# Kernel tuning notes

Measured on AMD Instinct MI355X. Metric: run time of the kernel, lower is better.

Reference implementation:

```python
import jax, jax.numpy as jnp
import numpy as np

N_NODES = 100000
DROP_P = 0.2


def _degree_norm(idx, n):
    deg = jax.ops.segment_sum(jnp.ones_like(idx, dtype=jnp.float32), idx, num_segments=n)
    return jnp.maximum(deg, 1.0) ** -0.5


def gcn_layer(x, src, dst, W, b, n):
    # DGL GraphConv, norm='both', in_feats > out_feats so weight is applied first.
    norm_src = _degree_norm(src, n)  # out-degree^{-1/2}
    norm_dst = _degree_norm(dst, n)  # in-degree^{-1/2}
    h = (x * norm_src[:, None]) @ W            # [N, d_out]
    agg = jax.ops.segment_sum(h[src], dst, num_segments=n)  # gather-scatter over edges
    return agg * norm_dst[:, None] + b


def setup_inputs() -> dict:
    key = jax.random.key(0)
    k = jax.random.split(key, 5)
    x = jax.random.normal(k[0], (N_NODES, 256), dtype=jnp.float32)
    edge_index = jax.random.randint(k[1], (2, 1600000), 0, N_NODES, dtype=jnp.int64)
    W1 = jax.random.normal(k[2], (256, 128), dtype=jnp.float32) * (1.0 / np.sqrt(256))
    b1 = jnp.zeros((128,), dtype=jnp.float32)
    W2 = jax.random.normal(k[3], (128, 47), dtype=jnp.float32) * (1.0 / np.sqrt(128))
    b2 = jnp.zeros((47,), dtype=jnp.float32)
    return {"x": x, "edge_index": edge_index, "W1": W1, "b1": b1, "W2": W2, "b2": b2}


def reference(x, edge_index, W1, b1, W2, b2):
    src, dst = edge_index[0], edge_index[1]
    n = x.shape[0]
    # CRD: GraphConv -> relu -> dropout (F.dropout default training=True; fixed mask)
    h = gcn_layer(x, src, dst, W1, b1, n)
    h = jax.nn.relu(h)
    keep = jax.random.bernoulli(jax.random.key(42), 1.0 - DROP_P, h.shape)
    h = jnp.where(keep, h / (1.0 - DROP_P), 0.0)
    # CLS: GraphConv -> log_softmax over class dim
    out = gcn_layer(h, src, dst, W2, b2, n)
    return jax.nn.log_softmax(out, axis=-1)
```

## Files before the change

kernel.cpp:

```cpp
#include <hip/hip_runtime.h>
#include <math.h>


#define NF0 256
#define NF1 128
#define NC  47
#define CB  1024

typedef __attribute__((ext_vector_type(8))) short bfrag;
typedef __attribute__((ext_vector_type(4))) float f32x4;

__device__ __forceinline__ unsigned short f2bf(float f) {
  unsigned u = __float_as_uint(f);
  return (unsigned short)((u + 0x7fffu + ((u >> 16) & 1u)) >> 16);
}
__device__ __forceinline__ unsigned pack2bf(float a, float b) {
  return (unsigned)f2bf(a) | ((unsigned)f2bf(b) << 16);
}
__device__ __forceinline__ float bflo(unsigned v) { return __uint_as_float(v << 16); }
__device__ __forceinline__ float bfhi(unsigned v) { return __uint_as_float(v & 0xffff0000u); }
__device__ __forceinline__ float bf2f(unsigned short b) {
  return __uint_as_float((unsigned)b << 16);
}

__device__ __forceinline__ unsigned rotl_(unsigned x, int n) {
  return (x << n) | (x >> (32 - n));
}
__device__ __forceinline__ void threefry2x32_(unsigned x0, unsigned x1,
                                              unsigned& o0, unsigned& o1) {
  const unsigned k0 = 0u, k1 = 42u;
  const unsigned k2 = k0 ^ k1 ^ 0x1BD11BDAu;
  x0 += k0; x1 += k1;
  x0+=x1; x1=rotl_(x1,13); x1^=x0;
  x0+=x1; x1=rotl_(x1,15); x1^=x0;
  x0+=x1; x1=rotl_(x1,26); x1^=x0;
  x0+=x1; x1=rotl_(x1, 6); x1^=x0;
  x0+=k1; x1+=k2+1u;
  x0+=x1; x1=rotl_(x1,17); x1^=x0;
  x0+=x1; x1=rotl_(x1,29); x1^=x0;
  x0+=x1; x1=rotl_(x1,16); x1^=x0;
  x0+=x1; x1=rotl_(x1,24); x1^=x0;
  x0+=k2; x1+=k0+2u;
  x0+=x1; x1=rotl_(x1,13); x1^=x0;
  x0+=x1; x1=rotl_(x1,15); x1^=x0;
  x0+=x1; x1=rotl_(x1,26); x1^=x0;
  x0+=x1; x1=rotl_(x1, 6); x1^=x0;
  x0+=k0; x1+=k1+3u;
  x0+=x1; x1=rotl_(x1,17); x1^=x0;
  x0+=x1; x1=rotl_(x1,29); x1^=x0;
  x0+=x1; x1=rotl_(x1,16); x1^=x0;
  x0+=x1; x1=rotl_(x1,24); x1^=x0;
  x0+=k1; x1+=k2+4u;
  x0+=x1; x1=rotl_(x1,13); x1^=x0;
  x0+=x1; x1=rotl_(x1,15); x1^=x0;
  x0+=x1; x1=rotl_(x1,26); x1^=x0;
  x0+=x1; x1=rotl_(x1, 6); x1^=x0;
  x0+=k2; x1+=k0+5u;
  o0 = x0; o1 = x1;
}
__device__ __forceinline__ float dropout_mul(int j) {
  unsigned o0, o1;
  threefry2x32_(0u, (unsigned)j, o0, o1);
  unsigned bits = o0 ^ o1;
  float u = __uint_as_float((bits >> 9) | 0x3f800000u) - 1.0f;
  return (u < 0.8f) ? 1.25f : 0.0f;
}


__global__ __launch_bounds__(256) void k_chist(const int* __restrict__ ei, int E,
                                               int nbk,
                                               unsigned* __restrict__ bCntD,
                                               unsigned* __restrict__ bCntS,
                                               const float* __restrict__ W1,
                                               const float* __restrict__ W2,
                                               unsigned* __restrict__ W1t32,
                                               unsigned* __restrict__ W2t32) {
  if (blockIdx.x >= 256) {
    int i = (blockIdx.x - 256) * 256 + threadIdx.x;
    if (i < 128 * 128) {
      int n = i >> 7, k = (i & 127) << 1;
      W1t32[i] = pack2bf(W1[(size_t)k * NF1 + n], W1[(size_t)(k + 1) * NF1 + n]);
    } else if (i < 128 * 128 + 48 * 64) {
      int j = i - 128 * 128;
      int f = j >> 6, k = (j & 63) << 1;
      float a = (f < NC) ? W2[(size_t)k * NC + f] : 0.f;
      float c = (f < NC) ? W2[(size_t)(k + 1) * NC + f] : 0.f;
      W2t32[j] = pack2bf(a, c);
    }
    return;
  }
  __shared__ unsigned hd[128], hs[128];
  for (int i = threadIdx.x; i < 128; i += 256) { hd[i] = 0; hs[i] = 0; }
  __syncthreads();
  for (int e = blockIdx.x * 256 + threadIdx.x; e < E; e += 256 * 256) {
    int s = ei[e], d = ei[E + e];
    atomicAdd(&hs[s >> 10], 1u);
    atomicAdd(&hd[d >> 10], 1u);
  }
  __syncthreads();
  for (int i = threadIdx.x; i < nbk; i += 256) {
    if (hd[i]) atomicAdd(&bCntD[i], hd[i]);
    if (hs[i]) atomicAdd(&bCntS[i], hs[i]);
  }
}

__global__ __launch_bounds__(256) void k_cscatter(const int* __restrict__ ei, int E,
                                                  const unsigned* __restrict__ bCntD,
                                                  const unsigned* __restrict__ bCntS,
                                                  unsigned* __restrict__ curD,
                                                  unsigned* __restrict__ curS,
                                                  unsigned* __restrict__ pd,
                                                  unsigned short* __restrict__ ps,
                                                  int nbk) {
  __shared__ unsigned hd[128], hs[128];
  __shared__ unsigned baseD[128], baseS[128];
  __shared__ unsigned sc[256];
  const int t = threadIdx.x;
  int per = (E + gridDim.x - 1) / gridDim.x;
  int e0 = blockIdx.x * per;
  int e1 = min(e0 + per, E);
  unsigned orig = (t < 128) ? ((t < nbk) ? bCntD[t] : 0u)
                            : (((t - 128) < nbk) ? bCntS[t - 128] : 0u);
  sc[t] = orig;
  if (t < 128) { hd[t] = 0; hs[t] = 0; }
  __syncthreads();
  for (int e = e0 + t; e < e1; e += 256) {
    int s = ei[e], d = ei[E + e];
    atomicAdd(&hs[s >> 10], 1u);
    atomicAdd(&hd[d >> 10], 1u);
  }
  __syncthreads();
  #pragma unroll
  for (int o = 1; o < 128; o <<= 1) {
    unsigned u = ((t & 127) >= o) ? sc[t - o] : 0u;
    __syncthreads();
    sc[t] += u;
    __syncthreads();
  }
  if (t < 128) {
    unsigned excl = sc[t] - orig;
    unsigned h = hd[t];
    baseD[t] = excl + (h ? atomicAdd(&curD[t], h) : 0u);
    hd[t] = 0;
  } else {
    int i = t - 128;
    unsigned excl = sc[t] - orig;
    unsigned h = hs[i];
    baseS[i] = excl + (h ? atomicAdd(&curS[i], h) : 0u);
    hs[i] = 0;
  }
  __syncthreads();
  for (int e = e0 + t; e < e1; e += 256) {
    int s = ei[e], d = ei[E + e];
    int bd = d >> 10, bs = s >> 10;
    unsigned pD = baseD[bd] + atomicAdd(&hd[bd], 1u);
    unsigned pS = baseS[bs] + atomicAdd(&hs[bs], 1u);
    pd[pD] = ((unsigned)(d & (CB - 1)) << 17) | (unsigned)s;
    ps[pS] = (unsigned short)(s & (CB - 1));
  }
}

__global__ __launch_bounds__(256) void k_fine(const unsigned* __restrict__ bCntD,
                                              const unsigned* __restrict__ bCntS,
                                              const unsigned* __restrict__ pd,
                                              const unsigned short* __restrict__ ps,
                                              unsigned* __restrict__ off,
                                              float* __restrict__ norm_dst,
                                              float* __restrict__ norm_src,
                                              int* __restrict__ csr,
                                              int N, int E, int nbk) {
  __shared__ unsigned cnt[CB];
  __shared__ unsigned part[256];
  __shared__ unsigned sc[256];
  const int t = threadIdx.x;
  const bool isD = (int)blockIdx.x < nbk;
  const int b = isD ? (int)blockIdx.x : ((int)blockIdx.x - nbk);
  unsigned orig = (t < 128) ? ((t < nbk) ? bCntD[t] : 0u)
                            : (((t - 128) < nbk) ? bCntS[t - 128] : 0u);
  sc[t] = orig;
  __syncthreads();
  #pragma unroll
  for (int o = 1; o < 128; o <<= 1) {
    unsigned u = ((t & 127) >= o) ? sc[t - o] : 0u;
    __syncthreads();
    sc[t] += u;
    __syncthreads();
  }
  const int idx = isD ? b : (128 + b);
  const unsigned hi = sc[idx];
  const unsigned lo = hi - (isD ? bCntD[b] : bCntS[b]);
  const int base = b << 10;
  for (int i = t; i < CB; i += 256) cnt[i] = 0;
  __syncthreads();
  if (isD) {
    for (unsigned j = lo + t; j < hi; j += 256) atomicAdd(&cnt[pd[j] >> 17], 1u);
    __syncthreads();
    unsigned c0 = cnt[4*t], c1 = cnt[4*t+1], c2 = cnt[4*t+2], c3 = cnt[4*t+3];
    unsigned tsum = c0 + c1 + c2 + c3;
    part[t] = tsum;
    __syncthreads();
    #pragma unroll
    for (int o = 1; o < 256; o <<= 1) {
      unsigned u = (t >= o) ? part[t - o] : 0u;
      __syncthreads();
      part[t] += u;
      __syncthreads();
    }
    unsigned e0 = part[t] - tsum;
    unsigned p0 = e0, p1 = e0 + c0, p2 = p1 + c1, p3 = p2 + c2;
    int n0 = base + 4 * t;
    if (n0 + 0 < N) { off[n0+0] = lo + p0; norm_dst[n0+0] = 1.0f / sqrtf((float)(c0 < 1u ? 1u : c0)); }
    if (n0 + 1 < N) { off[n0+1] = lo + p1; norm_dst[n0+1] = 1.0f / sqrtf((float)(c1 < 1u ? 1u : c1)); }
    if (n0 + 2 < N) { off[n0+2] = lo + p2; norm_dst[n0+2] = 1.0f / sqrtf((float)(c2 < 1u ? 1u : c2)); }
    if (n0 + 3 < N) { off[n0+3] = lo + p3; norm_dst[n0+3] = 1.0f / sqrtf((float)(c3 < 1u ? 1u : c3)); }
    if (b == nbk - 1 && t == 0) off[N] = (unsigned)E;
    __syncthreads();
    cnt[4*t] = p0; cnt[4*t+1] = p1; cnt[4*t+2] = p2; cnt[4*t+3] = p3;
    __syncthreads();
    for (unsigned j = lo + t; j < hi; j += 256) {
      unsigned v = pd[j];
      unsigned pos = atomicAdd(&cnt[v >> 17], 1u);
      csr[lo + pos] = (int)(v & 0x1FFFFu);
    }
  } else {
    for (unsigned j = lo + t; j < hi; j += 256) atomicAdd(&cnt[ps[j]], 1u);
    __syncthreads();
    for (int i = t; i < CB; i += 256) {
      int n = base + i;
      if (n < N) {
        unsigned c = cnt[i];
        norm_src[n] = 1.0f / sqrtf((float)(c < 1u ? 1u : c));
      }
    }
  }
}

__global__ __launch_bounds__(256) void k_gemm1(const float* __restrict__ x,
                                               const unsigned* __restrict__ W1t32,
                                               const float* __restrict__ norm_src,
                                               unsigned short* __restrict__ h1, int N) {
  __shared__ unsigned As[128][20];
  __shared__ unsigned Bs[128][20];
  const int m0 = blockIdx.x * 128;
  const int t = threadIdx.x;
  const int lane = t & 63, wid = t >> 6;
  const int fr = lane & 15, ko = (lane >> 4) * 8;

  f32x4 acc[2][8];
  #pragma unroll
  for (int r = 0; r < 2; r++)
    #pragma unroll
    for (int c = 0; c < 8; c++) acc[r][c] = (f32x4){0.f, 0.f, 0.f, 0.f};

  const int sr = t >> 1;
  const int shw = (t & 1) * 8;

  for (int k0 = 0; k0 < NF0; k0 += 32) {
    {
      unsigned w[8];
      int gm = m0 + sr;
      if (gm < N) {
        const float* p = x + (size_t)gm * NF0 + k0 + shw * 2;
        #pragma unroll
        for (int q = 0; q < 4; q++) {
          float4 v = *(const float4*)(p + q * 4);
          w[2*q]   = pack2bf(v.x, v.y);
          w[2*q+1] = pack2bf(v.z, v.w);
        }
      } else {
        #pragma unroll
        for (int q = 0; q < 8; q++) w[q] = 0u;
      }
      *(uint4*)&As[sr][shw]     = make_uint4(w[0], w[1], w[2], w[3]);
      *(uint4*)&As[sr][shw + 4] = make_uint4(w[4], w[5], w[6], w[7]);
    }
    {
      const unsigned* pb = W1t32 + (size_t)sr * (NF0 / 2) + (k0 >> 1) + shw;
      *(uint4*)&Bs[sr][shw]     = *(const uint4*)pb;
      *(uint4*)&Bs[sr][shw + 4] = *(const uint4*)(pb + 4);
    }
    __syncthreads();
    const unsigned short* As16 = (const unsigned short*)&As[0][0];
    const unsigned short* Bs16 = (const unsigned short*)&Bs[0][0];
    #pragma unroll
    for (int r = 0; r < 2; r++) {
      bfrag a = *(const bfrag*)(As16 + (size_t)(wid * 32 + r * 16 + fr) * 40 + ko);
      #pragma unroll
      for (int c = 0; c < 8; c++) {
        bfrag b = *(const bfrag*)(Bs16 + (size_t)(c * 16 + fr) * 40 + ko);
        acc[r][c] = __builtin_amdgcn_mfma_f32_16x16x32_bf16(a, b, acc[r][c], 0, 0, 0);
      }
    }
    __syncthreads();
  }

  #pragma unroll
  for (int r = 0; r < 2; r++) {
    int rbase = m0 + wid * 32 + r * 16 + (lane >> 4) * 4;
    float ns[4];
    #pragma unroll
    for (int g = 0; g < 4; g++) ns[g] = (rbase + g < N) ? norm_src[rbase + g] : 0.f;
    #pragma unroll
    for (int c = 0; c < 8; c++) {
      int col = c * 16 + fr;
      #pragma unroll
      for (int g = 0; g < 4; g++) {
        int row = rbase + g;
        if (row < N) h1[(size_t)row * NF1 + col] = f2bf(acc[r][c][g] * ns[g]);
      }
    }
  }
}

__global__ __launch_bounds__(256) void k_gather1(const unsigned* __restrict__ off,
                                                 const int* __restrict__ csr,
                                                 const unsigned short* __restrict__ h1,
                                                 const float* __restrict__ norm_dst,
                                                 const float* __restrict__ norm_src,
                                                 const float* __restrict__ b1,
                                                 unsigned* __restrict__ h2, int N) {
  const int t = threadIdx.x;
  const int lane = t & 63, wid = t >> 6;
  const int f = lane << 1;
  const int ngroups = (N + 3) >> 2;
  const float2 bb = *(const float2*)(b1 + f);

  for (int grp = blockIdx.x; grp < ngroups; grp += gridDim.x) {
    int node = grp * 4 + wid;
    if (node >= N) continue;
    unsigned j = off[node], e1 = off[node + 1];
    float ax = 0.f, ay = 0.f;
    for (; j + 4 <= e1; j += 4) {
      int s0 = csr[j], s1 = csr[j+1], s2 = csr[j+2], s3 = csr[j+3];
      unsigned v0 = *(const unsigned*)(h1 + (size_t)s0 * NF1 + f);
      unsigned v1 = *(const unsigned*)(h1 + (size_t)s1 * NF1 + f);
      unsigned v2 = *(const unsigned*)(h1 + (size_t)s2 * NF1 + f);
      unsigned v3 = *(const unsigned*)(h1 + (size_t)s3 * NF1 + f);
      ax += (bflo(v0) + bflo(v1)) + (bflo(v2) + bflo(v3));
      ay += (bfhi(v0) + bfhi(v1)) + (bfhi(v2) + bfhi(v3));
    }
    for (; j < e1; j++) {
      unsigned v = *(const unsigned*)(h1 + (size_t)csr[j] * NF1 + f);
      ax += bflo(v); ay += bfhi(v);
    }
    float nd = norm_dst[node], ns = norm_src[node];
    float v0 = fmaxf(ax * nd + bb.x, 0.f);
    float v1 = fmaxf(ay * nd + bb.y, 0.f);
    int jf = node * NF1 + f;
    v0 *= dropout_mul(jf) * ns;
    v1 *= dropout_mul(jf + 1) * ns;
    h2[(size_t)node * 64 + lane] = pack2bf(v0, v1);
  }
}

__global__ __launch_bounds__(256) void k_gemm2(const unsigned* __restrict__ h2,
                                               const unsigned* __restrict__ W2t32,
                                               unsigned short* __restrict__ g, int N) {
  const int t = threadIdx.x;
  const int lane = t & 63, wid = t >> 6;
  const int fr = lane & 15, hi4 = lane >> 4;
  const int row = blockIdx.x * 64 + wid * 16 + fr;

  bfrag a[4];
  const unsigned* ap = h2 + (size_t)row * 64 + hi4 * 4;
  #pragma unroll
  for (int kk = 0; kk < 4; kk++) {
    uint4 v = *(const uint4*)(ap + kk * 16);
    a[kk] = *(bfrag*)&v;
  }

  const int rbase = blockIdx.x * 64 + wid * 16 + hi4 * 4;
  #pragma unroll
  for (int c = 0; c < 3; c++) {
    f32x4 acc = (f32x4){0.f, 0.f, 0.f, 0.f};
    const unsigned* bp = W2t32 + (size_t)(c * 16 + fr) * 64 + hi4 * 4;
    #pragma unroll
    for (int kk = 0; kk < 4; kk++) {
      uint4 w = *(const uint4*)(bp + kk * 16);
      bfrag b = *(bfrag*)&w;
      acc = __builtin_amdgcn_mfma_f32_16x16x32_bf16(a[kk], b, acc, 0, 0, 0);
    }
    int col = c * 16 + fr;
    #pragma unroll
    for (int r = 0; r < 4; r++) {
      int nr = rbase + r;
      if (nr < N) g[(size_t)nr * 48 + col] = f2bf(acc[r]);
    }
  }
}

__global__ __launch_bounds__(256) void k_gather2(const unsigned* __restrict__ off,
                                                 const int* __restrict__ csr,
                                                 const unsigned short* __restrict__ g,
                                                 const float* __restrict__ norm_dst,
                                                 const float* __restrict__ b2,
                                                 float* __restrict__ out, int N) {
  int node = (blockIdx.x * 256 + threadIdx.x) >> 6;
  int lane = threadIdx.x & 63;
  if (node >= N) return;
  unsigned j = off[node], e1 = off[node + 1];
  float acc = 0.f;
  for (; j + 4 <= e1; j += 4) {
    int s0 = csr[j], s1 = csr[j+1], s2 = csr[j+2], s3 = csr[j+3];
    if (lane < 48) {
      float a0 = bf2f(g[(size_t)s0 * 48 + lane]);
      float a1 = bf2f(g[(size_t)s1 * 48 + lane]);
      float a2 = bf2f(g[(size_t)s2 * 48 + lane]);
      float a3 = bf2f(g[(size_t)s3 * 48 + lane]);
      acc += (a0 + a1) + (a2 + a3);
    }
  }
  for (; j < e1; j++) {
    if (lane < 48) acc += bf2f(g[(size_t)csr[j] * 48 + lane]);
  }
  float nd = norm_dst[node];
  float vr = 0.f, m = -INFINITY;
  if (lane < NC) {
    vr = acc * nd + b2[lane];
    m = vr;
  }
  #pragma unroll
  for (int o = 32; o; o >>= 1) m = fmaxf(m, __shfl_xor(m, o));
  float ex = (lane < NC) ? expf(vr - m) : 0.f;
  #pragma unroll
  for (int o = 32; o; o >>= 1) ex += __shfl_xor(ex, o);
  float ls = logf(ex);
  if (lane < NC) out[(size_t)node * NC + lane] = vr - m - ls;
}

extern "C" void kernel_launch(void* const* d_in, const int* in_sizes, int n_in,
                              void* d_out, int out_size, void* d_ws, size_t ws_size,
                              hipStream_t stream) {
  const float* x  = (const float*)d_in[0];
  const int*   ei = (const int*)d_in[1];
  const float* W1 = (const float*)d_in[2];
  const float* b1 = (const float*)d_in[3];
  const float* W2 = (const float*)d_in[4];
  const float* b2 = (const float*)d_in[5];
  float* out = (float*)d_out;

  const int N = in_sizes[0] / NF0;
  const int E = in_sizes[1] / 2;
  const int nbk = (N + CB - 1) / CB;
  const int Npad = (N + 63) & ~63;

  unsigned* ws = (unsigned*)d_ws;
  size_t o = 0;
  auto alloc = [&](size_t elems) { size_t p = o; o += (elems + 3) & ~(size_t)3; return p; };
  float*    norm_src = (float*)(ws + alloc(N));
  float*    norm_dst = (float*)(ws + alloc(N));
  unsigned* off      = ws + alloc(N + 1);
  unsigned* bCntD    = ws + alloc(128);
  unsigned* bCntS    = ws + alloc(128);
  unsigned* curD     = ws + alloc(128);
  unsigned* curS     = ws + alloc(128);
  unsigned* pd       = ws + alloc(E);
  unsigned short* ps = (unsigned short*)(ws + alloc(E / 2));
  int*      csr      = (int*)(ws + alloc(E));
  unsigned* W1t32    = ws + alloc(128 * 128);
  unsigned* W2t32    = ws + alloc(48 * 64);
  unsigned short* h1 = (unsigned short*)(ws + alloc((size_t)N * NF1 / 2));
  unsigned* h2       = ws + alloc((size_t)Npad * 64);
  unsigned short* gbuf;
  if ((size_t)E * 3 >= (size_t)N * 48) {
    gbuf = (unsigned short*)pd;
  } else {
    gbuf = (unsigned short*)(ws + alloc(((size_t)N * 48 + 1) / 2));
  }

  hipMemsetAsync(bCntD, 0, 512 * sizeof(unsigned), stream);

  int wblk = (128 * 128 + 48 * 64 + 255) / 256;
  k_chist<<<256 + wblk, 256, 0, stream>>>(ei, E, nbk, bCntD, bCntS, W1, W2, W1t32, W2t32);
  k_cscatter<<<256, 256, 0, stream>>>(ei, E, bCntD, bCntS, curD, curS, pd, ps, nbk);
  k_fine<<<2 * nbk, 256, 0, stream>>>(bCntD, bCntS, pd, ps, off, norm_dst, norm_src,
                                      csr, N, E, nbk);
  k_gemm1<<<(N + 127) / 128, 256, 0, stream>>>(x, W1t32, norm_src, h1, N);
  k_gather1<<<2048, 256, 0, stream>>>(off, csr, h1, norm_dst, norm_src, b1, h2, N);
  k_gemm2<<<Npad / 64, 256, 0, stream>>>(h2, W2t32, gbuf, N);
  k_gather2<<<((size_t)N * 64 + 255) / 256, 256, 0, stream>>>(
      off, csr, gbuf, norm_dst, b2, out, N);
}
```

Before: 466.9 us.

## Precompute dropout bitmask and gather rows with 16-byte loads across edge groups

Dropout bits are now generated once into a packed bitmask by extra blocks in the histogram kernel, so the threefry hash runs off the gather's critical path and overlaps with other early work. The first gather kernel now has each wavefront handle four edges at a time: each 16-lane group loads a full 256-byte source row with uint4 loads, and the partial sums are combined with cross-lane shuffles before one lane group applies bias, ReLU and dropout and writes the output. This replaces narrow 4-byte loads with wide loads, at the cost of shuffle reductions, idle lanes in the epilogue, and an extra mask buffer read.

```diff
diff --git a/kernel.cpp b/kernel.cpp
--- a/kernel.cpp
+++ b/kernel.cpp
@@ -58,23 +58,35 @@
   x0+=k2; x1+=k0+5u;
   o0 = x0; o1 = x1;
 }
-__device__ __forceinline__ float dropout_mul(int j) {
+__device__ __forceinline__ unsigned dropout_bit(unsigned j) {
   unsigned o0, o1;
-  threefry2x32_(0u, (unsigned)j, o0, o1);
+  threefry2x32_(0u, j, o0, o1);
   unsigned bits = o0 ^ o1;
   float u = __uint_as_float((bits >> 9) | 0x3f800000u) - 1.0f;
-  return (u < 0.8f) ? 1.25f : 0.0f;
+  return (u < 0.8f) ? 1u : 0u;
 }
 
 
 __global__ __launch_bounds__(256) void k_chist(const int* __restrict__ ei, int E,
-                                               int nbk,
+                                               int nbk, int N, int wblk,
                                                unsigned* __restrict__ bCntD,
                                                unsigned* __restrict__ bCntS,
                                                const float* __restrict__ W1,
                                                const float* __restrict__ W2,
                                                unsigned* __restrict__ W1t32,
-                                               unsigned* __restrict__ W2t32) {
+                                               unsigned* __restrict__ W2t32,
+                                               unsigned* __restrict__ bmask) {
+  if ((int)blockIdx.x >= 256 + wblk) {
+    int i = (blockIdx.x - 256 - wblk) * 256 + threadIdx.x;
+    if (i < 4 * N) {
+      unsigned w = 0;
+      #pragma unroll 4
+      for (int tbit = 0; tbit < 32; tbit++)
+        w |= dropout_bit(32u * (unsigned)i + (unsigned)tbit) << tbit;
+      bmask[i] = w;
+    }
+    return;
+  }
   if (blockIdx.x >= 256) {
     int i = (blockIdx.x - 256) * 256 + threadIdx.x;
     if (i < 128 * 128) {
@@ -318,38 +330,76 @@
                                                  const float* __restrict__ norm_dst,
                                                  const float* __restrict__ norm_src,
                                                  const float* __restrict__ b1,
+                                                 const unsigned* __restrict__ bmask,
                                                  unsigned* __restrict__ h2, int N) {
   const int t = threadIdx.x;
   const int lane = t & 63, wid = t >> 6;
-  const int f = lane << 1;
+  const int eg = lane >> 4;
+  const int q  = lane & 15;
   const int ngroups = (N + 3) >> 2;
-  const float2 bb = *(const float2*)(b1 + f);
+  const float4 bA = *(const float4*)(b1 + q * 8);
+  const float4 bB = *(const float4*)(b1 + q * 8 + 4);
 
   for (int grp = blockIdx.x; grp < ngroups; grp += gridDim.x) {
     int node = grp * 4 + wid;
     if (node >= N) continue;
     unsigned j = off[node], e1 = off[node + 1];
-    float ax = 0.f, ay = 0.f;
+    float ax0=0.f, ax1=0.f, ax2=0.f, ax3=0.f;
+    float ay0=0.f, ay1=0.f, ay2=0.f, ay3=0.f;
     for (; j + 4 <= e1; j += 4) {
-      int s0 = csr[j], s1 = csr[j+1], s2 = csr[j+2], s3 = csr[j+3];
-      unsigned v0 = *(const unsigned*)(h1 + (size_t)s0 * NF1 + f);
-      unsigned v1 = *(const unsigned*)(h1 + (size_t)s1 * NF1 + f);
-      unsigned v2 = *(const unsigned*)(h1 + (size_t)s2 * NF1 + f);
-      unsigned v3 = *(const unsigned*)(h1 + (size_t)s3 * NF1 + f);
-      ax += (bflo(v0) + bflo(v1)) + (bflo(v2) + bflo(v3));
-      ay += (bfhi(v0) + bfhi(v1)) + (bfhi(v2) + bfhi(v3));
-    }
-    for (; j < e1; j++) {
-      unsigned v = *(const unsigned*)(h1 + (size_t)csr[j] * NF1 + f);
-      ax += bflo(v); ay += bfhi(v);
-    }
-    float nd = norm_dst[node], ns = norm_src[node];
-    float v0 = fmaxf(ax * nd + bb.x, 0.f);
-    float v1 = fmaxf(ay * nd + bb.y, 0.f);
-    int jf = node * NF1 + f;
-    v0 *= dropout_mul(jf) * ns;
-    v1 *= dropout_mul(jf + 1) * ns;
-    h2[(size_t)node * 64 + lane] = pack2bf(v0, v1);
+      int s = csr[j + eg];
+      uint4 v = *(const uint4*)(h1 + (size_t)s * NF1 + q * 8);
+      ax0 += bflo(v.x); ay0 += bfhi(v.x);
+      ax1 += bflo(v.y); ay1 += bfhi(v.y);
+      ax2 += bflo(v.z); ay2 += bfhi(v.z);
+      ax3 += bflo(v.w); ay3 += bfhi(v.w);
+    }
+    if (j < e1) {
+      unsigned rem = e1 - j;
+      if ((unsigned)eg < rem) {
+        int s = csr[j + eg];
+        uint4 v = *(const uint4*)(h1 + (size_t)s * NF1 + q * 8);
+        ax0 += bflo(v.x); ay0 += bfhi(v.x);
+        ax1 += bflo(v.y); ay1 += bfhi(v.y);
+        ax2 += bflo(v.z); ay2 += bfhi(v.z);
+        ax3 += bflo(v.w); ay3 += bfhi(v.w);
+      }
+    }
+    ax0 += __shfl_xor(ax0, 16); ax0 += __shfl_xor(ax0, 32);
+    ay0 += __shfl_xor(ay0, 16); ay0 += __shfl_xor(ay0, 32);
+    ax1 += __shfl_xor(ax1, 16); ax1 += __shfl_xor(ax1, 32);
+    ay1 += __shfl_xor(ay1, 16); ay1 += __shfl_xor(ay1, 32);
+    ax2 += __shfl_xor(ax2, 16); ax2 += __shfl_xor(ax2, 32);
+    ay2 += __shfl_xor(ay2, 16); ay2 += __shfl_xor(ay2, 32);
+    ax3 += __shfl_xor(ax3, 16); ax3 += __shfl_xor(ax3, 32);
+    ay3 += __shfl_xor(ay3, 16); ay3 += __shfl_xor(ay3, 32);
+    if (eg == 0) {
+      float nd = norm_dst[node], ns = norm_src[node];
+      unsigned mw = bmask[node * 4 + (q >> 2)];
+      unsigned mb = (mw >> ((q & 3) * 8)) & 0xffu;
+      float v0 = fmaxf(ax0 * nd + bA.x, 0.f);
+      float v1 = fmaxf(ay0 * nd + bA.y, 0.f);
+      float v2 = fmaxf(ax1 * nd + bA.z, 0.f);
+      float v3 = fmaxf(ay1 * nd + bA.w, 0.f);
+      float v4 = fmaxf(ax2 * nd + bB.x, 0.f);
+      float v5 = fmaxf(ay2 * nd + bB.y, 0.f);
+      float v6 = fmaxf(ax3 * nd + bB.z, 0.f);
+      float v7 = fmaxf(ay3 * nd + bB.w, 0.f);
+      v0 *= ((mb >> 0) & 1 ? 1.25f : 0.f) * ns;
+      v1 *= ((mb >> 1) & 1 ? 1.25f : 0.f) * ns;
+      v2 *= ((mb >> 2) & 1 ? 1.25f : 0.f) * ns;
+      v3 *= ((mb >> 3) & 1 ? 1.25f : 0.f) * ns;
+      v4 *= ((mb >> 4) & 1 ? 1.25f : 0.f) * ns;
+      v5 *= ((mb >> 5) & 1 ? 1.25f : 0.f) * ns;
+      v6 *= ((mb >> 6) & 1 ? 1.25f : 0.f) * ns;
+      v7 *= ((mb >> 7) & 1 ? 1.25f : 0.f) * ns;
+      uint4 o;
+      o.x = pack2bf(v0, v1);
+      o.y = pack2bf(v2, v3);
+      o.z = pack2bf(v4, v5);
+      o.w = pack2bf(v6, v7);
+      *(uint4*)(h2 + (size_t)node * 64 + q * 4) = o;
+    }
   }
 }
 
@@ -454,6 +504,7 @@
   unsigned* bCntS    = ws + alloc(128);
   unsigned* curD     = ws + alloc(128);
   unsigned* curS     = ws + alloc(128);
+  unsigned* bmask    = ws + alloc((size_t)4 * N);
   unsigned* pd       = ws + alloc(E);
   unsigned short* ps = (unsigned short*)(ws + alloc(E / 2));
   int*      csr      = (int*)(ws + alloc(E));
@@ -471,12 +522,15 @@
   hipMemsetAsync(bCntD, 0, 512 * sizeof(unsigned), stream);
 
   int wblk = (128 * 128 + 48 * 64 + 255) / 256;
-  k_chist<<<256 + wblk, 256, 0, stream>>>(ei, E, nbk, bCntD, bCntS, W1, W2, W1t32, W2t32);
+  int mblk = (4 * N + 255) / 256;
+  k_chist<<<256 + wblk + mblk, 256, 0, stream>>>(ei, E, nbk, N, wblk, bCntD, bCntS,
+                                                 W1, W2, W1t32, W2t32, bmask);
   k_cscatter<<<256, 256, 0, stream>>>(ei, E, bCntD, bCntS, curD, curS, pd, ps, nbk);
   k_fine<<<2 * nbk, 256, 0, stream>>>(bCntD, bCntS, pd, ps, off, norm_dst, norm_src,
                                       csr, N, E, nbk);
   k_gemm1<<<(N + 127) / 128, 256, 0, stream>>>(x, W1t32, norm_src, h1, N);
-  k_gather1<<<2048, 256, 0, stream>>>(off, csr, h1, norm_dst, norm_src, b1, h2, N);
+  k_gather1<<<2048, 256, 0, stream>>>(off, csr, h1, norm_dst, norm_src, b1, bmask,
+                                      h2, N);
   k_gemm2<<<Npad / 64, 256, 0, stream>>>(h2, W2t32, gbuf, N);
   k_gather2<<<((size_t)N * 64 + 255) / 256, 256, 0, stream>>>(
       off, csr, gbuf, norm_dst, b2, out, N);
```

After: 471.7 us. About the same (+1.0%).
